# Kernel optimization log

Hardware: AMD Instinct MI355X
Metric: run time of the kernel (lower is better)

## Reference

```python
import jax, jax.numpy as jnp
import numpy as np

TAGSET = 128
B, T = 128, 1024


def setup_inputs() -> dict:
    key = jax.random.key(0)
    k1, k2, k3, k4, k5 = jax.random.split(key, 5)
    feats = jax.random.normal(k1, (B, T, TAGSET), dtype=jnp.float32)
    tags = jax.random.randint(k2, (B, T), 0, TAGSET, dtype=jnp.int64)
    mask = jnp.ones((B, T), dtype=bool)
    transitions = 0.01 * jax.random.normal(k3, (TAGSET, TAGSET), dtype=jnp.float32)
    start_transitions = 0.01 * jax.random.normal(k4, (TAGSET,), dtype=jnp.float32)
    stop_transitions = 0.01 * jax.random.normal(k5, (TAGSET,), dtype=jnp.float32)
    return {"feats": feats, "transitions": transitions,
            "start_transitions": start_transitions, "stop_transitions": stop_transitions,
            "tags": tags, "mask": mask}


def _forward_alg(feats, transitions, start_transitions, stop_transitions, mask):
    # feats: [B,T,K], mask: [B,T]
    fv0 = start_transitions + feats[:, 0]  # [B,K]

    def step(fv, xs):
        feat_t, mask_t = xs  # [B,K], [B]
        # prev-tag axis is last: fv[b, j] + transitions[i, j] + feat_t[b, i]
        score = fv[:, None, :] + transitions[None, :, :] + feat_t[:, :, None]  # [B,K,K]
        nxt = jax.nn.logsumexp(score, axis=-1)  # [B,K]
        fv = jnp.where(mask_t[:, None], nxt, fv)
        return fv, None

    xs = (jnp.swapaxes(feats[:, 1:], 0, 1), jnp.swapaxes(mask[:, 1:], 0, 1))
    fv, _ = jax.lax.scan(step, fv0, xs)
    return jax.nn.logsumexp(fv + stop_transitions, axis=-1)  # [B]


def _score_sentence(feats, transitions, start_transitions, stop_transitions, tags, mask):
    b, t = mask.shape
    trans_score = transitions[tags[:, 1:], tags[:, :-1]]  # [B,T-1]
    emit = jnp.take_along_axis(feats, tags[:, :, None], axis=2)[..., 0]  # [B,T]
    score = jnp.where(mask[:, 1:], trans_score + emit[:, 1:], 0.0).sum(-1)
    score = score + emit[:, 0] + start_transitions[tags[:, 0]]
    last_idx = mask.astype(jnp.int32).sum(-1) - 1  # [B]
    last_tags = tags[jnp.arange(b), last_idx]
    return score + stop_transitions[last_tags]


def reference(feats, transitions, start_transitions, stop_transitions, tags, mask):
    fwd = _forward_alg(feats, transitions, start_transitions, stop_transitions, mask)
    gold = _score_sentence(feats, transitions, start_transitions, stop_transitions, tags, mask)
    return (fwd - gold).mean()
```

## Files before the change

### kernel.cpp

```cpp
#include <hip/hip_runtime.h>
#include <hip/hip_bf16.h>

#define T_LEN 1024
#define NT 128
#define CHUNK 16
#define NCHUNK (T_LEN / CHUNK)

typedef short bf16x8 __attribute__((ext_vector_type(8)));
typedef float f32x4 __attribute__((ext_vector_type(4)));

__device__ __forceinline__ void gload16(const float* g, float* l) {
  __builtin_amdgcn_global_load_lds(
      (const __attribute__((address_space(1))) unsigned int*)g,
      (__attribute__((address_space(3))) unsigned int*)l, 16, 0, 0);
}

__device__ __forceinline__ short f2bf(float x) {
  __hip_bfloat16 h = __float2bfloat16(x);
  return *reinterpret_cast<short*>(&h);
}

__global__ __launch_bounds__(64, 1) void crf_forward_kernel(
    const float* __restrict__ feats, const float* __restrict__ trans,
    const float* __restrict__ start, const float* __restrict__ stop,
    float* __restrict__ fwd_out) {
  const int b = blockIdx.x;
  const int tid = (int)threadIdx.x;
  const int c = tid & 15;
  const int g = tid >> 4;

  __shared__ float fraw[2][CHUNK * NT];
  __shared__ float fexp[CHUNK * NT];

  const float* fb = feats + (size_t)b * T_LEN * NT;

  bf16x8 E[8][4];
  const int rbase = 32 * (c >> 2) + (c & 3);
#pragma unroll
  for (int mt = 0; mt < 8; ++mt) {
    const float* tr = trans + (size_t)(rbase + 4 * mt) * NT + 32 * g;
#pragma unroll
    for (int kt = 0; kt < 4; ++kt) {
      float4 e0 = *reinterpret_cast<const float4*>(tr + 8 * kt);
      float4 e1 = *reinterpret_cast<const float4*>(tr + 8 * kt + 4);
      bf16x8 f;
      f[0] = f2bf(__expf(e0.x)); f[1] = f2bf(__expf(e0.y));
      f[2] = f2bf(__expf(e0.z)); f[3] = f2bf(__expf(e0.w));
      f[4] = f2bf(__expf(e1.x)); f[5] = f2bf(__expf(e1.y));
      f[6] = f2bf(__expf(e1.z)); f[7] = f2bf(__expf(e1.w));
      E[mt][kt] = f;
    }
  }

  float sv[32];
#pragma unroll
  for (int m = 0; m < 8; ++m) {
    float4 s4 = *reinterpret_cast<const float4*>(start + 32 * g + 4 * m);
    sv[4 * m + 0] = s4.x; sv[4 * m + 1] = s4.y;
    sv[4 * m + 2] = s4.z; sv[4 * m + 3] = s4.w;
  }
  float st0 = start[0];

#define STAGE(ch, buf)                                                     \
  {                                                                        \
    _Pragma("unroll") for (int seg = 0; seg < 8; ++seg)                    \
        gload16(fb + (ch) * (CHUNK * NT) + seg * 256 + tid * 4,            \
                &fraw[buf][seg * 256 + tid * 4]);                          \
  }
#define EXPPASS(buf)                                                       \
  {                                                                        \
    _Pragma("unroll") for (int m8 = 0; m8 < 8; ++m8) {                     \
      float4 v =                                                           \
          *reinterpret_cast<const float4*>(&fraw[buf][m8 * 256 + tid * 4]);\
      float4 o;                                                            \
      o.x = __expf(v.x); o.y = __expf(v.y);                                \
      o.z = __expf(v.z); o.w = __expf(v.w);                                \
      *reinterpret_cast<float4*>(&fexp[m8 * 256 + tid * 4]) = o;           \
    }                                                                      \
  }

  STAGE(0, 0)
  STAGE(1, 1)
  asm volatile("s_waitcnt vmcnt(8)" ::: "memory");
  EXPPASS(0)

  float Cacc = st0 + fraw[0][0];
  float uf[32];
#pragma unroll
  for (int m = 0; m < 8; ++m) {
    float4 f4 = *reinterpret_cast<const float4*>(&fraw[0][32 * g + 4 * m]);
    uf[4 * m + 0] = __expf(sv[4 * m + 0] + f4.x - Cacc);
    uf[4 * m + 1] = __expf(sv[4 * m + 1] + f4.y - Cacc);
    uf[4 * m + 2] = __expf(sv[4 * m + 2] + f4.z - Cacc);
    uf[4 * m + 3] = __expf(sv[4 * m + 3] + f4.w - Cacc);
  }
  bf16x8 ub[4];
#pragma unroll
  for (int kt = 0; kt < 4; ++kt) {
    bf16x8 t;
#pragma unroll
    for (int e = 0; e < 8; ++e) t[e] = f2bf(uf[8 * kt + e]);
    ub[kt] = t;
  }

  const f32x4 zero4 = {0.f, 0.f, 0.f, 0.f};

#define STEP(frow)                                                          \
  {                                                                         \
    float4 ef[8];                                                           \
    _Pragma("unroll") for (int m = 0; m < 8; ++m) ef[m] =                   \
        *reinterpret_cast<const float4*>(&fexp[(frow) * NT + 32 * g + 4 * m]); \
    f32x4 acc[8];                                                           \
    _Pragma("unroll") for (int mt = 0; mt < 8; ++mt) acc[mt] =              \
        __builtin_amdgcn_mfma_f32_16x16x32_bf16(E[mt][0], ub[0], zero4, 0,  \
                                                0, 0);                      \
    _Pragma("unroll") for (int kt = 1; kt < 4; ++kt) {                      \
      _Pragma("unroll") for (int mt = 0; mt < 8; ++mt) acc[mt] =            \
          __builtin_amdgcn_mfma_f32_16x16x32_bf16(E[mt][kt], ub[kt],        \
                                                  acc[mt], 0, 0, 0);        \
    }                                                                       \
    float u0 = __uint_as_float(                                             \
        __builtin_amdgcn_readlane(__float_as_uint(acc[0][0]), 0));          \
    float s = __builtin_amdgcn_rcpf(u0);                                    \
    Cacc += __logf(u0);                                                     \
    _Pragma("unroll") for (int mt = 0; mt < 8; ++mt) {                      \
      uf[4 * mt + 0] = acc[mt][0] * s * ef[mt].x;                           \
      uf[4 * mt + 1] = acc[mt][1] * s * ef[mt].y;                           \
      uf[4 * mt + 2] = acc[mt][2] * s * ef[mt].z;                           \
      uf[4 * mt + 3] = acc[mt][3] * s * ef[mt].w;                           \
    }                                                                       \
    _Pragma("unroll") for (int kt = 0; kt < 4; ++kt) {                      \
      bf16x8 t;                                                             \
      _Pragma("unroll") for (int e = 0; e < 8; ++e)                         \
          t[e] = f2bf(uf[8 * kt + e]);                                      \
      ub[kt] = t;                                                           \
    }                                                                       \
  }

#pragma unroll 4
  for (int trow = 1; trow < CHUNK; ++trow) STEP(trow)

  for (int ch = 1; ch < NCHUNK; ++ch) {
    asm volatile("s_waitcnt vmcnt(0)" ::: "memory");
    const int buf = ch & 1;
    EXPPASS(buf)
    if (ch + 1 < NCHUNK) STAGE(ch + 1, buf ^ 1)
#pragma unroll 4
    for (int trow = 0; trow < CHUNK; ++trow) STEP(trow)
  }
#undef STEP
#undef STAGE
#undef EXPPASS

  float tot = 0.f;
#pragma unroll
  for (int m = 0; m < 8; ++m) {
    float4 s4 = *reinterpret_cast<const float4*>(stop + 32 * g + 4 * m);
    tot += uf[4 * m + 0] * __expf(s4.x) + uf[4 * m + 1] * __expf(s4.y) +
           uf[4 * m + 2] * __expf(s4.z) + uf[4 * m + 3] * __expf(s4.w);
  }
  tot += __shfl_xor(tot, 16);
  tot += __shfl_xor(tot, 32);
  if (tid == 0) fwd_out[b] = Cacc + __logf(tot);
}

__global__ __launch_bounds__(256) void crf_gold_kernel(
    const float* __restrict__ feats, const float* __restrict__ trans,
    const float* __restrict__ start, const float* __restrict__ stop,
    const int* __restrict__ tags, const float* __restrict__ fwd,
    float* __restrict__ diff) {
  const int b = blockIdx.x;
  const int tid = (int)threadIdx.x;
  const int lane = tid & 63;
  const int w = tid >> 6;
  const int* tg = tags + b * T_LEN;
  const float* fb = feats + (size_t)b * T_LEN * NT;

  float acc = 0.f;
  for (int s = tid; s < T_LEN; s += 256) {
    int cu = tg[s];
    acc += fb[s * NT + cu];
    if (s > 0) acc += trans[cu * NT + tg[s - 1]];
  }
#pragma unroll
  for (int off = 1; off <= 32; off <<= 1) acc += __shfl_xor(acc, off);
  __shared__ float wr[4];
  if (lane == 0) wr[w] = acc;
  __syncthreads();
  if (tid == 0) {
    float gold = (wr[0] + wr[1]) + (wr[2] + wr[3]) + start[tg[0]] +
                 stop[tg[T_LEN - 1]];
    diff[b] = fwd[b] - gold;
  }
}

__global__ __launch_bounds__(128) void crf_final_kernel(
    const float* __restrict__ diff, float* __restrict__ out) {
  const int tid = (int)threadIdx.x;
  const int lane = tid & 63;
  const int w = tid >> 6;
  float v = diff[tid];
#pragma unroll
  for (int off = 1; off <= 32; off <<= 1) v += __shfl_xor(v, off);
  __shared__ float wr[2];
  if (lane == 0) wr[w] = v;
  __syncthreads();
  if (tid == 0) out[0] = (wr[0] + wr[1]) * (1.0f / 128.0f);
}

extern "C" void kernel_launch(void* const* d_in, const int* in_sizes, int n_in,
                              void* d_out, int out_size, void* d_ws,
                              size_t ws_size, hipStream_t stream) {
  const float* feats = (const float*)d_in[0];
  const float* trans = (const float*)d_in[1];
  const float* start = (const float*)d_in[2];
  const float* stop = (const float*)d_in[3];
  const int* tags = (const int*)d_in[4];
  float* ws = (float*)d_ws;
  float* fwd = ws;
  float* diff = ws + 128;
  float* out = (float*)d_out;

  crf_forward_kernel<<<128, 64, 0, stream>>>(feats, trans, start, stop, fwd);
  crf_gold_kernel<<<128, 256, 0, stream>>>(feats, trans, start, stop, tags, fwd,
                                           diff);
  crf_final_kernel<<<1, 128, 0, stream>>>(diff, out);
}
```

Measured before the change: 527.1 us.

## Batch 16 sequences per MFMA scan wave and precompute exp(feats) in a separate kernel

The forward-scan kernel now handles 16 batch elements per 64-lane wave, one per MFMA column, so the 16x16 MFMA tiles carry 16 useful columns instead of mostly idle ones, and only 8 blocks are launched. A separate elementwise kernel first writes exp(feats) to workspace, and the scan loads those values from global memory into registers four steps ahead. Transitions are pre-scaled by 1/128 so renormalisation only happens every 8 steps, with the log offset added back at the end. The costs are a full extra write and read of exp(feats) through global memory, only 8 waves doing the serial scan, and a reliance on values staying within bf16 and float range between renormalisations.

```diff
diff --git a/kernel.cpp b/kernel.cpp
--- a/kernel.cpp
+++ b/kernel.cpp
@@ -3,36 +3,37 @@
 
 #define T_LEN 1024
 #define NT 128
-#define CHUNK 16
-#define NCHUNK (T_LEN / CHUNK)
+#define LOG128 4.852030263919617f
 
 typedef short bf16x8 __attribute__((ext_vector_type(8)));
 typedef float f32x4 __attribute__((ext_vector_type(4)));
-
-__device__ __forceinline__ void gload16(const float* g, float* l) {
-  __builtin_amdgcn_global_load_lds(
-      (const __attribute__((address_space(1))) unsigned int*)g,
-      (__attribute__((address_space(3))) unsigned int*)l, 16, 0, 0);
-}
 
 __device__ __forceinline__ short f2bf(float x) {
   __hip_bfloat16 h = __float2bfloat16(x);
   return *reinterpret_cast<short*>(&h);
 }
 
-__global__ __launch_bounds__(64, 1) void crf_forward_kernel(
-    const float* __restrict__ feats, const float* __restrict__ trans,
+__global__ __launch_bounds__(256) void crf_exp_kernel(
+    const float* __restrict__ in, float* __restrict__ out, int n4) {
+  int i = blockIdx.x * 256 + (int)threadIdx.x;
+  const int stride = gridDim.x * 256;
+  for (; i < n4; i += stride) {
+    float4 v = reinterpret_cast<const float4*>(in)[i];
+    float4 o;
+    o.x = __expf(v.x); o.y = __expf(v.y);
+    o.z = __expf(v.z); o.w = __expf(v.w);
+    reinterpret_cast<float4*>(out)[i] = o;
+  }
+}
+
+__global__ __launch_bounds__(64, 1) void crf_scan_kernel(
+    const float* __restrict__ fexpG, const float* __restrict__ trans,
     const float* __restrict__ start, const float* __restrict__ stop,
     float* __restrict__ fwd_out) {
-  const int b = blockIdx.x;
   const int tid = (int)threadIdx.x;
   const int c = tid & 15;
   const int g = tid >> 4;
-
-  __shared__ float fraw[2][CHUNK * NT];
-  __shared__ float fexp[CHUNK * NT];
-
-  const float* fb = feats + (size_t)b * T_LEN * NT;
+  const int b0 = blockIdx.x * 16;
 
   bf16x8 E[8][4];
   const int rbase = 32 * (c >> 2) + (c & 3);
@@ -44,55 +45,44 @@
       float4 e0 = *reinterpret_cast<const float4*>(tr + 8 * kt);
       float4 e1 = *reinterpret_cast<const float4*>(tr + 8 * kt + 4);
       bf16x8 f;
-      f[0] = f2bf(__expf(e0.x)); f[1] = f2bf(__expf(e0.y));
-      f[2] = f2bf(__expf(e0.z)); f[3] = f2bf(__expf(e0.w));
-      f[4] = f2bf(__expf(e1.x)); f[5] = f2bf(__expf(e1.y));
-      f[6] = f2bf(__expf(e1.z)); f[7] = f2bf(__expf(e1.w));
+      f[0] = f2bf(__expf(e0.x) * 0.0078125f);
+      f[1] = f2bf(__expf(e0.y) * 0.0078125f);
+      f[2] = f2bf(__expf(e0.z) * 0.0078125f);
+      f[3] = f2bf(__expf(e0.w) * 0.0078125f);
+      f[4] = f2bf(__expf(e1.x) * 0.0078125f);
+      f[5] = f2bf(__expf(e1.y) * 0.0078125f);
+      f[6] = f2bf(__expf(e1.z) * 0.0078125f);
+      f[7] = f2bf(__expf(e1.w) * 0.0078125f);
       E[mt][kt] = f;
     }
   }
 
-  float sv[32];
+  const float st0 = start[0];
+  const float* gp = fexpG + (size_t)(b0 + c) * (T_LEN * NT) + 32 * g;
+
+  float EF[4][32];
+#define LOADEF(slot, t_)                                                   \
+  {                                                                        \
+    _Pragma("unroll") for (int m = 0; m < 8; ++m) {                        \
+      float4 q =                                                           \
+          *reinterpret_cast<const float4*>(gp + (size_t)(t_)*NT + 4 * m);  \
+      EF[slot][4 * m + 0] = q.x; EF[slot][4 * m + 1] = q.y;                \
+      EF[slot][4 * m + 2] = q.z; EF[slot][4 * m + 3] = q.w;                \
+    }                                                                      \
+  }
+
+  LOADEF(0, 0)
+  float m0 = __shfl(EF[0][0], c);
+  float Kc = st0 + __logf(m0);
+  float r0 = __builtin_amdgcn_rcpf(m0);
+  float uf[32];
 #pragma unroll
   for (int m = 0; m < 8; ++m) {
     float4 s4 = *reinterpret_cast<const float4*>(start + 32 * g + 4 * m);
-    sv[4 * m + 0] = s4.x; sv[4 * m + 1] = s4.y;
-    sv[4 * m + 2] = s4.z; sv[4 * m + 3] = s4.w;
-  }
-  float st0 = start[0];
-
-#define STAGE(ch, buf)                                                     \
-  {                                                                        \
-    _Pragma("unroll") for (int seg = 0; seg < 8; ++seg)                    \
-        gload16(fb + (ch) * (CHUNK * NT) + seg * 256 + tid * 4,            \
-                &fraw[buf][seg * 256 + tid * 4]);                          \
-  }
-#define EXPPASS(buf)                                                       \
-  {                                                                        \
-    _Pragma("unroll") for (int m8 = 0; m8 < 8; ++m8) {                     \
-      float4 v =                                                           \
-          *reinterpret_cast<const float4*>(&fraw[buf][m8 * 256 + tid * 4]);\
-      float4 o;                                                            \
-      o.x = __expf(v.x); o.y = __expf(v.y);                                \
-      o.z = __expf(v.z); o.w = __expf(v.w);                                \
-      *reinterpret_cast<float4*>(&fexp[m8 * 256 + tid * 4]) = o;           \
-    }                                                                      \
-  }
-
-  STAGE(0, 0)
-  STAGE(1, 1)
-  asm volatile("s_waitcnt vmcnt(8)" ::: "memory");
-  EXPPASS(0)
-
-  float Cacc = st0 + fraw[0][0];
-  float uf[32];
-#pragma unroll
-  for (int m = 0; m < 8; ++m) {
-    float4 f4 = *reinterpret_cast<const float4*>(&fraw[0][32 * g + 4 * m]);
-    uf[4 * m + 0] = __expf(sv[4 * m + 0] + f4.x - Cacc);
-    uf[4 * m + 1] = __expf(sv[4 * m + 1] + f4.y - Cacc);
-    uf[4 * m + 2] = __expf(sv[4 * m + 2] + f4.z - Cacc);
-    uf[4 * m + 3] = __expf(sv[4 * m + 3] + f4.w - Cacc);
+    uf[4 * m + 0] = __expf(s4.x - st0) * EF[0][4 * m + 0] * r0;
+    uf[4 * m + 1] = __expf(s4.y - st0) * EF[0][4 * m + 1] * r0;
+    uf[4 * m + 2] = __expf(s4.z - st0) * EF[0][4 * m + 2] * r0;
+    uf[4 * m + 3] = __expf(s4.w - st0) * EF[0][4 * m + 3] * r0;
   }
   bf16x8 ub[4];
 #pragma unroll
@@ -102,14 +92,12 @@
     for (int e = 0; e < 8; ++e) t[e] = f2bf(uf[8 * kt + e]);
     ub[kt] = t;
   }
+  LOADEF(1, 1) LOADEF(2, 2) LOADEF(3, 3)
 
   const f32x4 zero4 = {0.f, 0.f, 0.f, 0.f};
 
-#define STEP(frow)                                                          \
+#define STEP(t_, SL, RN)                                                    \
   {                                                                         \
-    float4 ef[8];                                                           \
-    _Pragma("unroll") for (int m = 0; m < 8; ++m) ef[m] =                   \
-        *reinterpret_cast<const float4*>(&fexp[(frow) * NT + 32 * g + 4 * m]); \
     f32x4 acc[8];                                                           \
     _Pragma("unroll") for (int mt = 0; mt < 8; ++mt) acc[mt] =              \
         __builtin_amdgcn_mfma_f32_16x16x32_bf16(E[mt][0], ub[0], zero4, 0,  \
@@ -119,38 +107,37 @@
           __builtin_amdgcn_mfma_f32_16x16x32_bf16(E[mt][kt], ub[kt],        \
                                                   acc[mt], 0, 0, 0);        \
     }                                                                       \
-    float u0 = __uint_as_float(                                             \
-        __builtin_amdgcn_readlane(__float_as_uint(acc[0][0]), 0));          \
-    float s = __builtin_amdgcn_rcpf(u0);                                    \
-    Cacc += __logf(u0);                                                     \
+    float sc = 1.0f;                                                        \
+    if (RN) {                                                               \
+      float u0 = __shfl(acc[0][0], c);                                      \
+      sc = __builtin_amdgcn_rcpf(u0);                                       \
+      Kc += __logf(u0);                                                     \
+    }                                                                       \
     _Pragma("unroll") for (int mt = 0; mt < 8; ++mt) {                      \
-      uf[4 * mt + 0] = acc[mt][0] * s * ef[mt].x;                           \
-      uf[4 * mt + 1] = acc[mt][1] * s * ef[mt].y;                           \
-      uf[4 * mt + 2] = acc[mt][2] * s * ef[mt].z;                           \
-      uf[4 * mt + 3] = acc[mt][3] * s * ef[mt].w;                           \
+      _Pragma("unroll") for (int r = 0; r < 4; ++r) {                       \
+        float v = acc[mt][r] * EF[SL][4 * mt + r];                          \
+        if (RN) v = v * sc;                                                 \
+        uf[4 * mt + r] = v;                                                 \
+      }                                                                     \
     }                                                                       \
     _Pragma("unroll") for (int kt = 0; kt < 4; ++kt) {                      \
-      bf16x8 t;                                                             \
+      bf16x8 tt;                                                            \
       _Pragma("unroll") for (int e = 0; e < 8; ++e)                         \
-          t[e] = f2bf(uf[8 * kt + e]);                                      \
-      ub[kt] = t;                                                           \
-    }                                                                       \
-  }
-
-#pragma unroll 4
-  for (int trow = 1; trow < CHUNK; ++trow) STEP(trow)
-
-  for (int ch = 1; ch < NCHUNK; ++ch) {
-    asm volatile("s_waitcnt vmcnt(0)" ::: "memory");
-    const int buf = ch & 1;
-    EXPPASS(buf)
-    if (ch + 1 < NCHUNK) STAGE(ch + 1, buf ^ 1)
-#pragma unroll 4
-    for (int trow = 0; trow < CHUNK; ++trow) STEP(trow)
+          tt[e] = f2bf(uf[8 * kt + e]);                                     \
+      ub[kt] = tt;                                                          \
+    }                                                                       \
+    LOADEF(SL, (t_) + 4)                                                    \
+  }
+
+  STEP(1, 1, false) STEP(2, 2, false) STEP(3, 3, false) STEP(4, 0, false)
+  STEP(5, 1, false) STEP(6, 2, false) STEP(7, 3, false)
+  for (int tb = 8; tb < 1024; tb += 8) {
+    STEP(tb + 0, 0, true)  STEP(tb + 1, 1, false) STEP(tb + 2, 2, false)
+    STEP(tb + 3, 3, false) STEP(tb + 4, 0, false) STEP(tb + 5, 1, false)
+    STEP(tb + 6, 2, false) STEP(tb + 7, 3, false)
   }
 #undef STEP
-#undef STAGE
-#undef EXPPASS
+#undef LOADEF
 
   float tot = 0.f;
 #pragma unroll
@@ -161,7 +148,7 @@
   }
   tot += __shfl_xor(tot, 16);
   tot += __shfl_xor(tot, 32);
-  if (tid == 0) fwd_out[b] = Cacc + __logf(tot);
+  if (g == 0) fwd_out[b0 + c] = Kc + 1023.0f * LOG128 + __logf(tot);
 }
 
 __global__ __launch_bounds__(256) void crf_gold_kernel(
@@ -219,9 +206,12 @@
   float* ws = (float*)d_ws;
   float* fwd = ws;
   float* diff = ws + 128;
+  float* fexpG = ws + 256;
   float* out = (float*)d_out;
 
-  crf_forward_kernel<<<128, 64, 0, stream>>>(feats, trans, start, stop, fwd);
+  const int n4 = (128 * T_LEN * NT) / 4;
+  crf_exp_kernel<<<4096, 256, 0, stream>>>(feats, fexpG, n4);
+  crf_scan_kernel<<<8, 64, 0, stream>>>(fexpG, trans, start, stop, fwd);
   crf_gold_kernel<<<128, 256, 0, stream>>>(feats, trans, start, stop, tags, fwd,
                                            diff);
   crf_final_kernel<<<1, 128, 0, stream>>>(diff, out);
```

New measurement: 907.6 us. 72.2% more time.
